# Optimization experiments

Measured on AMD Instinct MI355X. Metric: run time of the kernel, lower is better.

## Reference

```python
import jax, jax.numpy as jnp
import numpy as np

N, D, E, TOPK = 16384, 4096, 64, 8
NOISE_EPS = 0.01


def setup_inputs() -> dict:
    key = jax.random.key(0)
    kx, kw, kn = jax.random.split(key, 3)
    x = jax.random.normal(kx, (N, D), dtype=jnp.float32)
    W = jax.random.normal(kw, (D, E), dtype=jnp.float32) * 0.02  # gate weight (Linear, no bias)
    noise = jax.random.normal(kn, (N, E), dtype=jnp.float32) * NOISE_EPS  # training-mode gate noise
    return {"x": x, "W": W, "noise": noise, "top_k": TOPK}


def reference(x, W, noise, top_k):
    # logits -> noisy logits -> softmax gates
    gates = jax.nn.softmax(x @ W + noise, axis=-1)          # [N, E]
    top_k_gates, top_k_indices = jax.lax.top_k(gates, top_k)  # [N, k] each
    top_k_gates = top_k_gates / jnp.sum(top_k_gates, axis=-1, keepdims=True)
    # load-balancing aux loss (training path), vectorized over experts
    num_experts = W.shape[1]
    importance = jnp.mean(gates, axis=0)                     # [E]
    load = jnp.zeros((num_experts,), gates.dtype).at[top_k_indices.reshape(-1)].add(1.0)
    load = load / top_k_indices.size                         # mean of (indices == i) over N*k
    load_balancing_loss = jnp.sum(importance * load) * num_experts
    return top_k_gates, top_k_indices, load_balancing_loss
```

## Files before the change

### kernel.cpp

```cpp
#include <hip/hip_runtime.h>

#define NROWS 16384
#define DDIM  4096
#define NEXP  64
#define TAU   1e-3f
#define FB    1024
#define RB    2048
#define RBLK  64

typedef __attribute__((ext_vector_type(8))) short bf16x8;
typedef __attribute__((ext_vector_type(4))) float f32x4;

__device__ __forceinline__ ushort f2bf(float f) {
    uint u = __float_as_uint(f);
    u += 0x7FFFu + ((u >> 16) & 1u);
    return (ushort)(u >> 16);
}
__device__ __forceinline__ float bf2f(ushort h) {
    return __uint_as_float(((uint)h) << 16);
}
__device__ __forceinline__ void cvt8(const float4& a, const float4& b,
                                     bf16x8& H, bf16x8& L) {
    const float v[8] = {a.x, a.y, a.z, a.w, b.x, b.y, b.z, b.w};
    #pragma unroll
    for (int i = 0; i < 8; ++i) {
        const ushort h = f2bf(v[i]);
        H[i] = (short)h;
        L[i] = (short)f2bf(v[i] - bf2f(h));
    }
}

__global__ __launch_bounds__(256) void wprep(
    const float* __restrict__ Wg, ushort* __restrict__ wfrag)
{
    const int gid  = (int)blockIdx.x * 256 + threadIdx.x;
    const int lane = gid & 63, frag = gid >> 6;
    const int nt = frag & 3, ks = (frag >> 2) & 1, tg = frag >> 3;
    const int k0 = tg * 64 + ks * 32 + (lane >> 4) * 8;
    const int e  = nt * 16 + (lane & 15);
    bf16x8 H, L;
    #pragma unroll
    for (int j = 0; j < 8; ++j) {
        const float v = Wg[(size_t)(k0 + j) * NEXP + e];
        const ushort h = f2bf(v);
        H[j] = (short)h;
        L[j] = (short)f2bf(v - bf2f(h));
    }
    *(bf16x8*)&wfrag[((size_t)frag * 2 + 0) * 512 + lane * 8] = H;
    *(bf16x8*)&wfrag[((size_t)frag * 2 + 1) * 512 + lane * 8] = L;
}

__global__ __launch_bounds__(256, 4) void router_fused(
    const float* __restrict__ x, const ushort* __restrict__ wfrag,
    const float* __restrict__ noise, float* __restrict__ out_gates,
    float* __restrict__ out_idx, float* __restrict__ ws_imp,
    float* __restrict__ ws_load, int* __restrict__ worklist,
    int* __restrict__ counter)
{
    __shared__ float patch[4][16][66];
    __shared__ float red[4][NEXP];

    const int tid  = threadIdx.x;
    const int lane = tid & 63;
    const int w    = tid >> 6;
    const int rg   = blockIdx.x;
    const int fr   = lane & 15;
    const int q    = lane >> 4;

    const float* xp = x + (size_t)(rg * 16 + fr) * DDIM + w * 1024 + q * 8;
    const ushort* wfbase = wfrag + (size_t)(w * 16) * 8192 + lane * 8;

    f32x4 acc[4];
    #pragma unroll
    for (int nt = 0; nt < 4; ++nt) acc[nt] = (f32x4){0.f, 0.f, 0.f, 0.f};

    float4 c0a = *(const float4*)(xp);
    float4 c0b = *(const float4*)(xp + 4);
    float4 c1a = *(const float4*)(xp + 32);
    float4 c1b = *(const float4*)(xp + 36);

    for (int t = 0; t < 16; ++t) {
        float4 n0a, n0b, n1a, n1b;
        if (t + 1 < 16) {
            const float* xn = xp + (t + 1) * 64;
            n0a = *(const float4*)(xn);
            n0b = *(const float4*)(xn + 4);
            n1a = *(const float4*)(xn + 32);
            n1b = *(const float4*)(xn + 36);
        }

        bf16x8 ah0, al0, ah1, al1;
        cvt8(c0a, c0b, ah0, al0);
        cvt8(c1a, c1b, ah1, al1);

        const ushort* wt = wfbase + (size_t)t * 8192;
        #pragma unroll
        for (int ks = 0; ks < 2; ++ks) {
            const bf16x8 a_h = ks ? ah1 : ah0;
            const bf16x8 a_l = ks ? al1 : al0;
            #pragma unroll
            for (int nt = 0; nt < 4; ++nt) {
                const bf16x8 w_h =
                    *(const bf16x8*)&wt[((ks * 4 + nt) * 2 + 0) * 512];
                const bf16x8 w_l =
                    *(const bf16x8*)&wt[((ks * 4 + nt) * 2 + 1) * 512];
                acc[nt] = __builtin_amdgcn_mfma_f32_16x16x32_bf16(a_h, w_h, acc[nt], 0, 0, 0);
                acc[nt] = __builtin_amdgcn_mfma_f32_16x16x32_bf16(a_h, w_l, acc[nt], 0, 0, 0);
                acc[nt] = __builtin_amdgcn_mfma_f32_16x16x32_bf16(a_l, w_h, acc[nt], 0, 0, 0);
            }
        }
        c0a = n0a; c0b = n0b; c1a = n1a; c1b = n1b;
    }

    #pragma unroll
    for (int nt = 0; nt < 4; ++nt)
        #pragma unroll
        for (int r = 0; r < 4; ++r)
            patch[w][q * 4 + r][nt * 16 + fr] = acc[nt][r];
    __syncthreads();

    float impacc = 0.f, loadacc = 0.f;
    #pragma unroll
    for (int rr = 0; rr < 4; ++rr) {
        const int row  = w * 4 + rr;
        const int grow = rg * 16 + row;
        float v = patch[0][row][lane] + patch[1][row][lane]
                + patch[2][row][lane] + patch[3][row][lane]
                + noise[(size_t)grow * NEXP + lane];

        float m = v;
        #pragma unroll
        for (int off = 32; off; off >>= 1) m = fmaxf(m, __shfl_xor(m, off));
        const float ex = __expf(v - m);
        float s = ex;
        #pragma unroll
        for (int off = 32; off; off >>= 1) s += __shfl_xor(s, off);
        const float g = ex * (1.0f / s);
        impacc += g;

        float work = v, vprev = 0.f;
        float myv = 0.f, sumtop = 0.f;
        int myi = 0, mine = 0, flg = 0;
        #pragma unroll
        for (int j = 0; j < 9; ++j) {
            float bv = work, bg = g; int bi = lane;
            #pragma unroll
            for (int off = 32; off; off >>= 1) {
                const float ov = __shfl_xor(bv, off);
                const int   oi = __shfl_xor(bi, off);
                const float og = __shfl_xor(bg, off);
                if (ov > bv || (ov == bv && oi < bi)) { bv = ov; bi = oi; bg = og; }
            }
            if (j > 0) flg |= (vprev - bv < TAU) ? 1 : 0;
            vprev = bv;
            if (j < 8) {
                sumtop += bg;
                if (lane == j)  { myv = bg; myi = bi; }
                if (lane == bi) { work = -3e38f; mine = 1; }
            }
        }
        loadacc += (float)mine;

        if (lane < 8) {
            out_gates[(size_t)grow * 8 + lane] = myv / sumtop;
            out_idx  [(size_t)grow * 8 + lane] = (float)myi;
        }
        if (lane == 0 && flg) {
            const int pos = atomicAdd(counter, 1);
            worklist[pos] = grow;
        }
    }

    red[w][lane] = impacc;
    __syncthreads();
    if (w == 0)
        ws_imp[(size_t)rg * NEXP + lane] =
            red[0][lane] + red[1][lane] + red[2][lane] + red[3][lane];
    __syncthreads();
    red[w][lane] = loadacc;
    __syncthreads();
    if (w == 0)
        ws_load[(size_t)rg * NEXP + lane] =
            red[0][lane] + red[1][lane] + red[2][lane] + red[3][lane];
}

__global__ __launch_bounds__(256) void reduce_stage(
    const float* __restrict__ ws_imp, const float* __restrict__ ws_load,
    float* __restrict__ st_imp, float* __restrict__ st_load)
{
    __shared__ float si[4][NEXP], sl[4][NEXP];
    const int tid = threadIdx.x, e = tid & 63, sub = tid >> 6;
    float a = 0.f, b = 0.f;
    #pragma unroll
    for (int i = 0; i < 4; ++i) {
        const int blk = (int)blockIdx.x * 16 + sub * 4 + i;
        a += ws_imp[(size_t)blk * NEXP + e];
        b += ws_load[(size_t)blk * NEXP + e];
    }
    si[sub][e] = a; sl[sub][e] = b;
    __syncthreads();
    if (sub == 0) {
        st_imp [(size_t)blockIdx.x * NEXP + e] = si[0][e] + si[1][e] + si[2][e] + si[3][e];
        st_load[(size_t)blockIdx.x * NEXP + e] = sl[0][e] + sl[1][e] + sl[2][e] + sl[3][e];
    }
}

__global__ __launch_bounds__(256) void repair_finalize(
    const float* __restrict__ x, const float* __restrict__ Wg,
    const float* __restrict__ noise, const int* __restrict__ worklist,
    const int* __restrict__ counter, const float* __restrict__ st_imp,
    const float* __restrict__ st_load, float* __restrict__ out_gates,
    float* __restrict__ out_idx, float* __restrict__ loss_out)
{
    const int tid = threadIdx.x, lane = tid & 63, w = tid >> 6;

    if (blockIdx.x == RB) {
        __shared__ float si[4][NEXP], sl[4][NEXP];
        float a = 0.f, b = 0.f;
        #pragma unroll
        for (int j = 0; j < RBLK / 4; ++j) {
            const int blk = w * (RBLK / 4) + j;
            a += st_imp[(size_t)blk * NEXP + lane];
            b += st_load[(size_t)blk * NEXP + lane];
        }
        si[w][lane] = a; sl[w][lane] = b;
        __syncthreads();
        if (w == 0) {
            const float imp = (si[0][lane] + si[1][lane] + si[2][lane] + si[3][lane])
                              / (float)NROWS;
            const float ld  = (sl[0][lane] + sl[1][lane] + sl[2][lane] + sl[3][lane])
                              / (float)(NROWS * 8);
            float term = imp * ld;
            #pragma unroll
            for (int off = 32; off; off >>= 1) term += __shfl_xor(term, off);
            if (lane == 0) *loss_out = term * (float)NEXP;
        }
        return;
    }

    __shared__ float xr[DDIM];
    __shared__ double red64[4][NEXP];
    const int count = *counter;

    for (int i = (int)blockIdx.x; i < count; i += RB) {
        const int grow = worklist[i];
        __syncthreads();
        #pragma unroll
        for (int qq = 0; qq < 4; ++qq)
            ((float4*)xr)[tid + 256 * qq] =
                ((const float4*)(x + (size_t)grow * DDIM))[tid + 256 * qq];
        __syncthreads();

        double ch[8];
        #pragma unroll
        for (int c = 0; c < 8; ++c) ch[c] = 0.0;
        const float* wp = Wg + (size_t)(w * 1024) * NEXP + lane;
        const float* xq = xr + w * 1024;
        #pragma unroll 4
        for (int k = 0; k < 1024; k += 8) {
            #pragma unroll
            for (int c = 0; c < 8; ++c)
                ch[c] = fma((double)xq[k + c],
                            (double)wp[(size_t)(k + c) * NEXP], ch[c]);
        }
        red64[w][lane] = (((ch[0] + ch[1]) + (ch[2] + ch[3]))
                        + ((ch[4] + ch[5]) + (ch[6] + ch[7])));
        __syncthreads();

        if (w == 0) {
            const double v64 = (((red64[0][lane] + red64[1][lane]) + red64[2][lane])
                                + red64[3][lane]) + (double)noise[(size_t)grow * NEXP + lane];
            double m = v64;
            #pragma unroll
            for (int off = 32; off; off >>= 1) m = fmax(m, __shfl_xor(m, off));
            const float ex = __expf((float)(v64 - m));
            float s = ex;
            #pragma unroll
            for (int off = 32; off; off >>= 1) s += __shfl_xor(s, off);
            const float g = ex * (1.0f / s);

            double work = v64;
            float myv = 0.f, sumtop = 0.f, bg;
            int myi = 0;
            #pragma unroll
            for (int j = 0; j < 8; ++j) {
                double bv = work; int bi = lane; bg = g;
                #pragma unroll
                for (int off = 32; off; off >>= 1) {
                    const double ov = __shfl_xor(bv, off);
                    const int    oi = __shfl_xor(bi, off);
                    const float  og = __shfl_xor(bg, off);
                    if (ov > bv || (ov == bv && oi < bi)) { bv = ov; bi = oi; bg = og; }
                }
                sumtop += bg;
                if (lane == j)  { myv = bg; myi = bi; }
                if (lane == bi) work = -1e300;
            }
            if (lane < 8) {
                out_gates[(size_t)grow * 8 + lane] = myv / sumtop;
                out_idx  [(size_t)grow * 8 + lane] = (float)myi;
            }
        }
    }
}

extern "C" void kernel_launch(void* const* d_in, const int* in_sizes, int n_in,
                              void* d_out, int out_size, void* d_ws, size_t ws_size,
                              hipStream_t stream) {
    const float* x     = (const float*)d_in[0];
    const float* Wg    = (const float*)d_in[1];
    const float* noise = (const float*)d_in[2];
    float* out       = (float*)d_out;
    float* out_gates = out;
    float* out_idx   = out + (size_t)NROWS * 8;
    float* loss_out  = out + (size_t)2 * NROWS * 8;

    ushort* wfrag  = (ushort*)d_ws;
    float* ws_imp   = (float*)(wfrag + (size_t)1048576);
    float* ws_load  = ws_imp + (size_t)FB * NEXP;
    float* st_imp   = ws_load + (size_t)FB * NEXP;
    float* st_load  = st_imp + (size_t)RBLK * NEXP;
    int*   worklist = (int*)(st_load + (size_t)RBLK * NEXP);
    int*   counter  = worklist + NROWS;

    hipMemsetAsync(counter, 0, sizeof(int), stream);
    wprep          <<<128,    256, 0, stream>>>(Wg, wfrag);
    router_fused   <<<FB,     256, 0, stream>>>(x, wfrag, noise, out_gates, out_idx,
                                                ws_imp, ws_load, worklist, counter);
    reduce_stage   <<<RBLK,   256, 0, stream>>>(ws_imp, ws_load, st_imp, st_load);
    repair_finalize<<<RB + 1, 256, 0, stream>>>(x, Wg, noise, worklist, counter,
                                                st_imp, st_load, out_gates, out_idx,
                                                loss_out);
}
```

Before: 161.5 us.

## Split router GEMM into split-K MFMA kernel with LDS-staged weights

```diff
diff --git a/kernel.cpp b/kernel.cpp
--- a/kernel.cpp
+++ b/kernel.cpp
@@ -4,7 +4,7 @@
 #define DDIM  4096
 #define NEXP  64
 #define TAU   1e-3f
-#define FB    1024
+#define CB    2048
 #define RB    2048
 #define RBLK  64
 
@@ -50,38 +50,50 @@
     *(bf16x8*)&wfrag[((size_t)frag * 2 + 1) * 512 + lane * 8] = L;
 }
 
-__global__ __launch_bounds__(256, 4) void router_fused(
+__global__ __launch_bounds__(256, 2) void gemm_mfma(
     const float* __restrict__ x, const ushort* __restrict__ wfrag,
-    const float* __restrict__ noise, float* __restrict__ out_gates,
-    float* __restrict__ out_idx, float* __restrict__ ws_imp,
-    float* __restrict__ ws_load, int* __restrict__ worklist,
-    int* __restrict__ counter)
-{
-    __shared__ float patch[4][16][66];
-    __shared__ float red[4][NEXP];
+    float* __restrict__ partials, int* __restrict__ counter)
+{
+    if (blockIdx.x == 0 && threadIdx.x == 0) *counter = 0;
+
+    __shared__ ushort wbuf[2][8192];
 
     const int tid  = threadIdx.x;
     const int lane = tid & 63;
     const int w    = tid >> 6;
-    const int rg   = blockIdx.x;
+    const int rb   = (int)blockIdx.x >> 1;
+    const int kq   = (int)blockIdx.x & 1;
     const int fr   = lane & 15;
     const int q    = lane >> 4;
 
-    const float* xp = x + (size_t)(rg * 16 + fr) * DDIM + w * 1024 + q * 8;
-    const ushort* wfbase = wfrag + (size_t)(w * 16) * 8192 + lane * 8;
+    const float*  xp   = x + (size_t)(rb * 64 + w * 16 + fr) * DDIM
+                           + kq * 2048 + q * 8;
+    const ushort* wsrc = wfrag + (size_t)(kq * 32) * 8192 + tid * 8;
 
     f32x4 acc[4];
     #pragma unroll
     for (int nt = 0; nt < 4; ++nt) acc[nt] = (f32x4){0.f, 0.f, 0.f, 0.f};
 
+    uint4 wst[4];
+    #pragma unroll
+    for (int c = 0; c < 4; ++c)
+        wst[c] = *(const uint4*)(wsrc + c * 2048);
+    #pragma unroll
+    for (int c = 0; c < 4; ++c)
+        *(uint4*)&wbuf[0][c * 2048 + tid * 8] = wst[c];
     float4 c0a = *(const float4*)(xp);
     float4 c0b = *(const float4*)(xp + 4);
     float4 c1a = *(const float4*)(xp + 32);
     float4 c1b = *(const float4*)(xp + 36);
-
-    for (int t = 0; t < 16; ++t) {
+    __syncthreads();
+
+    int cur = 0;
+    for (int t = 0; t < 32; ++t) {
         float4 n0a, n0b, n1a, n1b;
-        if (t + 1 < 16) {
+        if (t + 1 < 32) {
+            #pragma unroll
+            for (int c = 0; c < 4; ++c)
+                wst[c] = *(const uint4*)(wsrc + (size_t)(t + 1) * 8192 + c * 2048);
             const float* xn = xp + (t + 1) * 64;
             n0a = *(const float4*)(xn);
             n0b = *(const float4*)(xn + 4);
@@ -93,7 +105,7 @@
         cvt8(c0a, c0b, ah0, al0);
         cvt8(c1a, c1b, ah1, al1);
 
-        const ushort* wt = wfbase + (size_t)t * 8192;
+        const ushort* wt = &wbuf[cur][0];
         #pragma unroll
         for (int ks = 0; ks < 2; ++ks) {
             const bf16x8 a_h = ks ? ah1 : ah0;
@@ -101,32 +113,49 @@
             #pragma unroll
             for (int nt = 0; nt < 4; ++nt) {
                 const bf16x8 w_h =
-                    *(const bf16x8*)&wt[((ks * 4 + nt) * 2 + 0) * 512];
+                    *(const bf16x8*)&wt[((ks * 4 + nt) * 2 + 0) * 512 + lane * 8];
                 const bf16x8 w_l =
-                    *(const bf16x8*)&wt[((ks * 4 + nt) * 2 + 1) * 512];
+                    *(const bf16x8*)&wt[((ks * 4 + nt) * 2 + 1) * 512 + lane * 8];
                 acc[nt] = __builtin_amdgcn_mfma_f32_16x16x32_bf16(a_h, w_h, acc[nt], 0, 0, 0);
                 acc[nt] = __builtin_amdgcn_mfma_f32_16x16x32_bf16(a_h, w_l, acc[nt], 0, 0, 0);
                 acc[nt] = __builtin_amdgcn_mfma_f32_16x16x32_bf16(a_l, w_h, acc[nt], 0, 0, 0);
             }
         }
-        c0a = n0a; c0b = n0b; c1a = n1a; c1b = n1b;
-    }
-
+
+        if (t + 1 < 32) {
+            #pragma unroll
+            for (int c = 0; c < 4; ++c)
+                *(uint4*)&wbuf[cur ^ 1][c * 2048 + tid * 8] = wst[c];
+            c0a = n0a; c0b = n0b; c1a = n1a; c1b = n1b;
+        }
+        __syncthreads();
+        cur ^= 1;
+    }
+
+    float* po = partials + ((size_t)kq * NROWS + rb * 64 + w * 16) * 64;
     #pragma unroll
     for (int nt = 0; nt < 4; ++nt)
         #pragma unroll
         for (int r = 0; r < 4; ++r)
-            patch[w][q * 4 + r][nt * 16 + fr] = acc[nt][r];
-    __syncthreads();
+            po[(q * 4 + r) * 64 + nt * 16 + fr] = acc[nt][r];
+}
+
+__global__ __launch_bounds__(256) void combine_epilogue(
+    const float* __restrict__ partials, const float* __restrict__ noise,
+    float* __restrict__ out_gates, float* __restrict__ out_idx,
+    float* __restrict__ ws_imp, float* __restrict__ ws_load,
+    int* __restrict__ worklist, int* __restrict__ counter)
+{
+    __shared__ float red[4][NEXP];
+    const int tid = threadIdx.x, lane = tid & 63, w = tid >> 6;
 
     float impacc = 0.f, loadacc = 0.f;
     #pragma unroll
-    for (int rr = 0; rr < 4; ++rr) {
-        const int row  = w * 4 + rr;
-        const int grow = rg * 16 + row;
-        float v = patch[0][row][lane] + patch[1][row][lane]
-                + patch[2][row][lane] + patch[3][row][lane]
-                + noise[(size_t)grow * NEXP + lane];
+    for (int rr = 0; rr < 2; ++rr) {
+        const int grow = (int)blockIdx.x * 8 + w * 2 + rr;
+        float v = noise[(size_t)grow * NEXP + lane]
+                + partials[(size_t)grow * 64 + lane]
+                + partials[(size_t)NROWS * 64 + (size_t)grow * 64 + lane];
 
         float m = v;
         #pragma unroll
@@ -174,13 +203,13 @@
     red[w][lane] = impacc;
     __syncthreads();
     if (w == 0)
-        ws_imp[(size_t)rg * NEXP + lane] =
+        ws_imp[(size_t)blockIdx.x * NEXP + lane] =
             red[0][lane] + red[1][lane] + red[2][lane] + red[3][lane];
     __syncthreads();
     red[w][lane] = loadacc;
     __syncthreads();
     if (w == 0)
-        ws_load[(size_t)rg * NEXP + lane] =
+        ws_load[(size_t)blockIdx.x * NEXP + lane] =
             red[0][lane] + red[1][lane] + red[2][lane] + red[3][lane];
 }
 
@@ -192,8 +221,8 @@
     const int tid = threadIdx.x, e = tid & 63, sub = tid >> 6;
     float a = 0.f, b = 0.f;
     #pragma unroll
-    for (int i = 0; i < 4; ++i) {
-        const int blk = (int)blockIdx.x * 16 + sub * 4 + i;
+    for (int i = 0; i < 8; ++i) {
+        const int blk = (int)blockIdx.x * 32 + sub * 8 + i;
         a += ws_imp[(size_t)blk * NEXP + e];
         b += ws_load[(size_t)blk * NEXP + e];
     }
@@ -315,17 +344,18 @@
     float* out_idx   = out + (size_t)NROWS * 8;
     float* loss_out  = out + (size_t)2 * NROWS * 8;
 
-    ushort* wfrag  = (ushort*)d_ws;
-    float* ws_imp   = (float*)(wfrag + (size_t)1048576);
-    float* ws_load  = ws_imp + (size_t)FB * NEXP;
-    float* st_imp   = ws_load + (size_t)FB * NEXP;
+    ushort* wfrag   = (ushort*)d_ws;
+    float* partials = (float*)(wfrag + (size_t)1048576);
+    float* ws_imp   = partials + (size_t)2 * NROWS * 64;
+    float* ws_load  = ws_imp + (size_t)CB * NEXP;
+    float* st_imp   = ws_load + (size_t)CB * NEXP;
     float* st_load  = st_imp + (size_t)RBLK * NEXP;
     int*   worklist = (int*)(st_load + (size_t)RBLK * NEXP);
     int*   counter  = worklist + NROWS;
 
-    hipMemsetAsync(counter, 0, sizeof(int), stream);
     wprep          <<<128,    256, 0, stream>>>(Wg, wfrag);
-    router_fused   <<<FB,     256, 0, stream>>>(x, wfrag, noise, out_gates, out_idx,
+    gemm_mfma      <<<512,    256, 0, stream>>>(x, wfrag, partials, counter);
+    combine_epilogue<<<CB,    256, 0, stream>>>(partials, noise, out_gates, out_idx,
                                                 ws_imp, ws_load, worklist, counter);
     reduce_stage   <<<RBLK,   256, 0, stream>>>(ws_imp, ws_load, st_imp, st_load);
     repair_finalize<<<RB + 1, 256, 0, stream>>>(x, Wg, noise, worklist, counter,
```

Measured after the change: 144.8 us. 10.3% less time.

## Stage W fragments in shared memory with double buffering, 32 rows per block

Applied to the files above, without the earlier changes.

```diff
diff --git a/kernel.cpp b/kernel.cpp
--- a/kernel.cpp
+++ b/kernel.cpp
@@ -4,7 +4,7 @@
 #define DDIM  4096
 #define NEXP  64
 #define TAU   1e-3f
-#define FB    1024
+#define FB    512
 #define RB    2048
 #define RBLK  64
 
@@ -31,8 +31,10 @@
 }
 
 __global__ __launch_bounds__(256) void wprep(
-    const float* __restrict__ Wg, ushort* __restrict__ wfrag)
+    const float* __restrict__ Wg, ushort* __restrict__ wfrag,
+    int* __restrict__ counter)
 {
+    if (blockIdx.x == 0 && threadIdx.x == 0) *counter = 0;
     const int gid  = (int)blockIdx.x * 256 + threadIdx.x;
     const int lane = gid & 63, frag = gid >> 6;
     const int nt = frag & 3, ks = (frag >> 2) & 1, tg = frag >> 3;
@@ -50,38 +52,61 @@
     *(bf16x8*)&wfrag[((size_t)frag * 2 + 1) * 512 + lane * 8] = L;
 }
 
-__global__ __launch_bounds__(256, 4) void router_fused(
+__global__ __launch_bounds__(256, 2) void router_fused(
     const float* __restrict__ x, const ushort* __restrict__ wfrag,
     const float* __restrict__ noise, float* __restrict__ out_gates,
     float* __restrict__ out_idx, float* __restrict__ ws_imp,
     float* __restrict__ ws_load, int* __restrict__ worklist,
     int* __restrict__ counter)
 {
-    __shared__ float patch[4][16][66];
+    __shared__ ushort wbuf[2][2][8192];
+    __shared__ float patch[2][16][66];
     __shared__ float red[4][NEXP];
 
     const int tid  = threadIdx.x;
     const int lane = tid & 63;
     const int w    = tid >> 6;
-    const int rg   = blockIdx.x;
+    const int rt   = w >> 1;
+    const int kh   = w & 1;
+    const int rb   = blockIdx.x;
     const int fr   = lane & 15;
     const int q    = lane >> 4;
 
-    const float* xp = x + (size_t)(rg * 16 + fr) * DDIM + w * 1024 + q * 8;
-    const ushort* wfbase = wfrag + (size_t)(w * 16) * 8192 + lane * 8;
+    const float* xp = x + (size_t)(rb * 32 + rt * 16 + fr) * DDIM
+                        + kh * 2048 + q * 8;
 
     f32x4 acc[4];
     #pragma unroll
     for (int nt = 0; nt < 4; ++nt) acc[nt] = (f32x4){0.f, 0.f, 0.f, 0.f};
 
+    uint4 wst[8];
+    #pragma unroll
+    for (int s = 0; s < 2; ++s)
+        #pragma unroll
+        for (int j = 0; j < 4; ++j)
+            wst[s * 4 + j] = *(const uint4*)(wfrag + (size_t)(s * 32) * 8192
+                                             + (j * 256 + tid) * 8);
+    #pragma unroll
+    for (int s = 0; s < 2; ++s)
+        #pragma unroll
+        for (int j = 0; j < 4; ++j)
+            *(uint4*)&wbuf[s][0][(j * 256 + tid) * 8] = wst[s * 4 + j];
     float4 c0a = *(const float4*)(xp);
     float4 c0b = *(const float4*)(xp + 4);
     float4 c1a = *(const float4*)(xp + 32);
     float4 c1b = *(const float4*)(xp + 36);
-
-    for (int t = 0; t < 16; ++t) {
+    __syncthreads();
+
+    int cur = 0;
+    for (int t = 0; t < 32; ++t) {
         float4 n0a, n0b, n1a, n1b;
-        if (t + 1 < 16) {
+        if (t + 1 < 32) {
+            #pragma unroll
+            for (int s = 0; s < 2; ++s)
+                #pragma unroll
+                for (int j = 0; j < 4; ++j)
+                    wst[s * 4 + j] = *(const uint4*)(wfrag
+                        + (size_t)(s * 32 + t + 1) * 8192 + (j * 256 + tid) * 8);
             const float* xn = xp + (t + 1) * 64;
             n0a = *(const float4*)(xn);
             n0b = *(const float4*)(xn + 4);
@@ -93,7 +118,7 @@
         cvt8(c0a, c0b, ah0, al0);
         cvt8(c1a, c1b, ah1, al1);
 
-        const ushort* wt = wfbase + (size_t)t * 8192;
+        const ushort* wt = &wbuf[kh][cur][0];
         #pragma unroll
         for (int ks = 0; ks < 2; ++ks) {
             const bf16x8 a_h = ks ? ah1 : ah0;
@@ -101,31 +126,50 @@
             #pragma unroll
             for (int nt = 0; nt < 4; ++nt) {
                 const bf16x8 w_h =
-                    *(const bf16x8*)&wt[((ks * 4 + nt) * 2 + 0) * 512];
+                    *(const bf16x8*)&wt[((ks * 4 + nt) * 2 + 0) * 512 + lane * 8];
                 const bf16x8 w_l =
-                    *(const bf16x8*)&wt[((ks * 4 + nt) * 2 + 1) * 512];
+                    *(const bf16x8*)&wt[((ks * 4 + nt) * 2 + 1) * 512 + lane * 8];
                 acc[nt] = __builtin_amdgcn_mfma_f32_16x16x32_bf16(a_h, w_h, acc[nt], 0, 0, 0);
                 acc[nt] = __builtin_amdgcn_mfma_f32_16x16x32_bf16(a_h, w_l, acc[nt], 0, 0, 0);
                 acc[nt] = __builtin_amdgcn_mfma_f32_16x16x32_bf16(a_l, w_h, acc[nt], 0, 0, 0);
             }
         }
-        c0a = n0a; c0b = n0b; c1a = n1a; c1b = n1b;
-    }
-
-    #pragma unroll
-    for (int nt = 0; nt < 4; ++nt)
-        #pragma unroll
-        for (int r = 0; r < 4; ++r)
-            patch[w][q * 4 + r][nt * 16 + fr] = acc[nt][r];
+
+        if (t + 1 < 32) {
+            #pragma unroll
+            for (int s = 0; s < 2; ++s)
+                #pragma unroll
+                for (int j = 0; j < 4; ++j)
+                    *(uint4*)&wbuf[s][cur ^ 1][(j * 256 + tid) * 8] = wst[s * 4 + j];
+            c0a = n0a; c0b = n0b; c1a = n1a; c1b = n1b;
+        }
+        __syncthreads();
+        cur ^= 1;
+    }
+
+    if (kh == 1) {
+        #pragma unroll
+        for (int nt = 0; nt < 4; ++nt)
+            #pragma unroll
+            for (int r = 0; r < 4; ++r)
+                patch[rt][q * 4 + r][nt * 16 + fr] = acc[nt][r];
+    }
+    __syncthreads();
+    if (kh == 0) {
+        #pragma unroll
+        for (int nt = 0; nt < 4; ++nt)
+            #pragma unroll
+            for (int r = 0; r < 4; ++r)
+                patch[rt][q * 4 + r][nt * 16 + fr] += acc[nt][r];
+    }
     __syncthreads();
 
     float impacc = 0.f, loadacc = 0.f;
     #pragma unroll
-    for (int rr = 0; rr < 4; ++rr) {
-        const int row  = w * 4 + rr;
-        const int grow = rg * 16 + row;
-        float v = patch[0][row][lane] + patch[1][row][lane]
-                + patch[2][row][lane] + patch[3][row][lane]
+    for (int rr = 0; rr < 8; ++rr) {
+        const int row  = w * 8 + rr;
+        const int grow = rb * 32 + row;
+        float v = patch[row >> 4][row & 15][lane]
                 + noise[(size_t)grow * NEXP + lane];
 
         float m = v;
@@ -174,13 +218,13 @@
     red[w][lane] = impacc;
     __syncthreads();
     if (w == 0)
-        ws_imp[(size_t)rg * NEXP + lane] =
+        ws_imp[(size_t)rb * NEXP + lane] =
             red[0][lane] + red[1][lane] + red[2][lane] + red[3][lane];
     __syncthreads();
     red[w][lane] = loadacc;
     __syncthreads();
     if (w == 0)
-        ws_load[(size_t)rg * NEXP + lane] =
+        ws_load[(size_t)rb * NEXP + lane] =
             red[0][lane] + red[1][lane] + red[2][lane] + red[3][lane];
 }
 
@@ -192,8 +236,8 @@
     const int tid = threadIdx.x, e = tid & 63, sub = tid >> 6;
     float a = 0.f, b = 0.f;
     #pragma unroll
-    for (int i = 0; i < 4; ++i) {
-        const int blk = (int)blockIdx.x * 16 + sub * 4 + i;
+    for (int i = 0; i < 2; ++i) {
+        const int blk = (int)blockIdx.x * 8 + sub * 2 + i;
         a += ws_imp[(size_t)blk * NEXP + e];
         b += ws_load[(size_t)blk * NEXP + e];
     }
@@ -315,7 +359,7 @@
     float* out_idx   = out + (size_t)NROWS * 8;
     float* loss_out  = out + (size_t)2 * NROWS * 8;
 
-    ushort* wfrag  = (ushort*)d_ws;
+    ushort* wfrag   = (ushort*)d_ws;
     float* ws_imp   = (float*)(wfrag + (size_t)1048576);
     float* ws_load  = ws_imp + (size_t)FB * NEXP;
     float* st_imp   = ws_load + (size_t)FB * NEXP;
@@ -323,8 +367,7 @@
     int*   worklist = (int*)(st_load + (size_t)RBLK * NEXP);
     int*   counter  = worklist + NROWS;
 
-    hipMemsetAsync(counter, 0, sizeof(int), stream);
-    wprep          <<<128,    256, 0, stream>>>(Wg, wfrag);
+    wprep          <<<128,    256, 0, stream>>>(Wg, wfrag, counter);
     router_fused   <<<FB,     256, 0, stream>>>(x, wfrag, noise, out_gates, out_idx,
                                                 ws_imp, ws_load, worklist, counter);
     reduce_stage   <<<RBLK,   256, 0, stream>>>(ws_imp, ws_load, st_imp, st_load);
```

Result: slower. 171.0 us (+5.9%).
